# Kernel tuning notes

Measured on AMD Instinct MI355X. Metric: run time of the kernel, lower is better.

## Reference

```python
import jax, jax.numpy as jnp
import numpy as np

B, S, H, I, E = 1, 2048, 2048, 5632, 8
JITTER = 0.01
NEG = jnp.float32(-1e30)  # stands in for -inf; softmax prob underflows to 0


def setup_inputs() -> dict:
    key = jax.random.key(0)
    ks = jax.random.split(key, 5)
    return {
        "hidden_states": jax.random.normal(ks[0], (B, S, H), jnp.float32),
        "gate_w": jax.random.normal(ks[1], (E, H), jnp.float32) * 0.02,   # nn.Linear(H, E) weight
        "w1": jax.random.normal(ks[2], (E, I, H), jnp.float32) * 0.02,    # per-expert w1 weight [out=I, in=H]
        "w2": jax.random.normal(ks[3], (E, H, I), jnp.float32) * 0.02,    # per-expert w2 weight [out=H, in=I]
        "w3": jax.random.normal(ks[4], (E, I, H), jnp.float32) * 0.02,    # per-expert w3 weight [out=I, in=H]
    }


def _sparsemixer_top2(scores, jitter_eps):
    # masked_sampling_omp_inference: sparse-mixer top-2 routing
    top2, sel = jax.lax.top_k(scores, 2)                      # [T,2], [T,2]
    e = scores.shape[-1]
    # --- first expert multiplier ---
    m1 = top2[:, 0:1]                                         # [T,1]
    factor1 = jnp.maximum(jnp.abs(scores), m1)                # clamp(|s|, min=m1)
    mask1 = (m1 - scores) / factor1 > 2.0 * jitter_eps
    p1 = jax.nn.softmax(jnp.where(mask1, NEG, scores), axis=-1)
    mult1 = jnp.take_along_axis(p1, sel[:, 0:1], axis=-1)     # [T,1]
    # --- second expert multiplier (first expert knocked out) ---
    m2 = top2[:, 1:2]
    factor2 = jnp.maximum(jnp.abs(scores), m2)
    mask2 = (m2 - scores) / factor2 > 2.0 * jitter_eps
    onehot0 = sel[:, 0:1] == jnp.arange(e)[None, :]           # scatter(-inf) at top-1 index
    p2 = jax.nn.softmax(jnp.where(onehot0 | mask2, NEG, scores), axis=-1)
    mult2 = jnp.take_along_axis(p2, sel[:, 1:2], axis=-1)     # [T,1]
    return jnp.concatenate([mult1, mult2], axis=-1), sel       # [T,2], [T,2]


def reference(hidden_states, gate_w, w1, w2, w3):
    b, s, h = hidden_states.shape
    x = hidden_states.reshape(-1, h)                          # [T,H]
    logits = x @ gate_w.T                                     # [T,E] router logits
    mult, sel = _sparsemixer_top2(logits, JITTER)
    out = jnp.zeros_like(x)
    for e in range(w1.shape[0]):                              # fixed small expert count
        # combined routing weight for expert e (0 if not selected)
        we = jnp.sum(jnp.where(sel == e, mult, 0.0), axis=-1)  # [T]
        hid = jax.nn.silu(x @ w1[e].T) * (x @ w3[e].T)        # SwiGLU [T,I]
        out = out + we[:, None] * (hid @ w2[e].T)
    return out.reshape(b, s, h)
```

## Files before the change

### kernel.cpp

```cpp
#include <hip/hip_runtime.h>

#define TOKENS 2048
#define HDIM   2048
#define IDIM   5632
#define NEXP   8
#define NSLOT  (TOKENS * 2)
#define BM 128
#define BN 128
#define BK 32

typedef __attribute__((ext_vector_type(8))) short bf16x8;
typedef __attribute__((ext_vector_type(4))) float f32x4;

__device__ __forceinline__ unsigned short f2bf(float f) {
    union { float f; unsigned u; } v; v.f = f;
    unsigned r = v.u + 0x7FFFu + ((v.u >> 16) & 1u);
    return (unsigned short)(r >> 16);
}
__device__ __forceinline__ unsigned pack2(float lo, float hi) {
    return (unsigned)f2bf(lo) | ((unsigned)f2bf(hi) << 16);
}
__device__ __forceinline__ void stage_b_chunk(const float* __restrict__ p, unsigned short* dst) {
    float4 lo = *(const float4*)(p);
    float4 hi = *(const float4*)(p + 4);
    uint4 v;
    v.x = pack2(lo.x, lo.y);
    v.y = pack2(lo.z, lo.w);
    v.z = pack2(hi.x, hi.y);
    v.w = pack2(hi.z, hi.w);
    *(uint4*)dst = v;
}

__global__ __launch_bounds__(256) void k_zero(float* __restrict__ out) {
    int i = blockIdx.x * 256 + threadIdx.x;
    float4 z = {0.f, 0.f, 0.f, 0.f};
    ((float4*)out)[i] = z;
}

__global__ __launch_bounds__(256) void k_gate(const float* __restrict__ x,
                                              const float* __restrict__ gw,
                                              int* __restrict__ sel,
                                              float* __restrict__ wts) {
    int wave = threadIdx.x >> 6, lane = threadIdx.x & 63;
    int t = blockIdx.x * 4 + wave;
    const float4* xr = (const float4*)(x + (size_t)t * HDIM);
    const float4* g  = (const float4*)gw;
    float acc[NEXP];
#pragma unroll
    for (int e = 0; e < NEXP; e++) acc[e] = 0.f;
#pragma unroll
    for (int it = 0; it < HDIM / 4 / 64; ++it) {
        int idx = it * 64 + lane;
        float4 xv = xr[idx];
#pragma unroll
        for (int e = 0; e < NEXP; e++) {
            float4 gv = g[e * (HDIM / 4) + idx];
            acc[e] += xv.x * gv.x + xv.y * gv.y + xv.z * gv.z + xv.w * gv.w;
        }
    }
#pragma unroll
    for (int e = 0; e < NEXP; e++) {
        float v = acc[e];
#pragma unroll
        for (int off = 32; off > 0; off >>= 1) v += __shfl_xor(v, off, 64);
        acc[e] = v;
    }
    if (lane == 0) {
        float s[NEXP];
#pragma unroll
        for (int e = 0; e < NEXP; e++) s[e] = acc[e];
        float m1 = s[0]; int i1 = 0;
#pragma unroll
        for (int e = 1; e < NEXP; e++) if (s[e] > m1) { m1 = s[e]; i1 = e; }
        float m2 = -3.0e38f; int i2 = 0;
#pragma unroll
        for (int e = 0; e < NEXP; e++) if (e != i1 && s[e] > m2) { m2 = s[e]; i2 = e; }
        float sum1 = 0.f;
#pragma unroll
        for (int e = 0; e < NEXP; e++) {
            float f = fmaxf(fabsf(s[e]), m1);
            bool masked = ((m1 - s[e]) / f) > 0.02f;
            if (!masked) sum1 += expf(s[e] - m1);
        }
        float sum2 = 0.f;
#pragma unroll
        for (int e = 0; e < NEXP; e++) {
            if (e == i1) continue;
            float f = fmaxf(fabsf(s[e]), m2);
            bool masked = ((m2 - s[e]) / f) > 0.02f;
            if (!masked) sum2 += expf(s[e] - m2);
        }
        sel[2 * t]     = i1;
        sel[2 * t + 1] = i2;
        wts[2 * t]     = 1.f / sum1;
        wts[2 * t + 1] = 1.f / sum2;
    }
}

__global__ __launch_bounds__(256) void k_hist(const int* __restrict__ sel,
                                              int* __restrict__ cnt,
                                              int* __restrict__ offs,
                                              int* __restrict__ cursor) {
    __shared__ int c_s[NEXP];
    int tid = threadIdx.x;
    if (tid < NEXP) c_s[tid] = 0;
    __syncthreads();
    for (int i = tid; i < NSLOT; i += 256) atomicAdd(&c_s[sel[i]], 1);
    __syncthreads();
    if (tid == 0) {
        int o = 0;
        for (int e = 0; e < NEXP; e++) { cnt[e] = c_s[e]; offs[e] = o; o += c_s[e]; cursor[e] = 0; }
    }
}

__global__ __launch_bounds__(256) void k_gather(const float* __restrict__ x,
                                                const int* __restrict__ sel,
                                                const float* __restrict__ wts,
                                                const int* __restrict__ offs,
                                                int* __restrict__ cursor,
                                                int* __restrict__ rowtok,
                                                float* __restrict__ roww,
                                                unsigned short* __restrict__ Xe) {
    int t = blockIdx.x;
    __shared__ int slot_s[2];
    if (threadIdx.x == 0) {
        int s0 = sel[2 * t], s1 = sel[2 * t + 1];
        int p0 = offs[s0] + atomicAdd(&cursor[s0], 1);
        int p1 = offs[s1] + atomicAdd(&cursor[s1], 1);
        rowtok[p0] = t; roww[p0] = wts[2 * t];
        rowtok[p1] = t; roww[p1] = wts[2 * t + 1];
        slot_s[0] = p0; slot_s[1] = p1;
    }
    __syncthreads();
    int p0 = slot_s[0], p1 = slot_s[1];
    int base = threadIdx.x * 8;
    const float* xp = x + (size_t)t * HDIM + base;
    float4 a = *(const float4*)(xp);
    float4 b = *(const float4*)(xp + 4);
    uint4 v;
    v.x = pack2(a.x, a.y); v.y = pack2(a.z, a.w);
    v.z = pack2(b.x, b.y); v.w = pack2(b.z, b.w);
    *(uint4*)(Xe + (size_t)p0 * HDIM + base) = v;
    *(uint4*)(Xe + (size_t)p1 * HDIM + base) = v;
}

__global__ __launch_bounds__(256, 2) void k_ffn1(const unsigned short* __restrict__ Xe,
                                                 const float* __restrict__ w1,
                                                 const float* __restrict__ w3,
                                                 const int* __restrict__ cnt,
                                                 const int* __restrict__ offs,
                                                 unsigned short* __restrict__ hid) {
    int e = blockIdx.z;
    int c = cnt[e];
    int bm = blockIdx.y;
    if (bm * BM >= c) return;
    int n0 = blockIdx.x * BN;
    int row0 = offs[e] + bm * BM;
    int rows_here = c - bm * BM;
    const float* W1 = w1 + (size_t)e * IDIM * HDIM;
    const float* W3 = w3 + (size_t)e * IDIM * HDIM;

    __shared__ __align__(16) unsigned short As[8 * 512];
    __shared__ __align__(16) unsigned short B1s[8 * 512];
    __shared__ __align__(16) unsigned short B3s[8 * 512];

    int tid = threadIdx.x, lane = tid & 63, wave = tid >> 6;
    int wm = wave >> 1, wn = wave & 1;
    int fr = lane & 15, kq = lane >> 4;

    f32x4 acc1[4][4], acc3[4][4];
    f32x4 z = {0.f, 0.f, 0.f, 0.f};
#pragma unroll
    for (int i = 0; i < 4; i++)
#pragma unroll
        for (int j = 0; j < 4; j++) { acc1[i][j] = z; acc3[i][j] = z; }

    int ar0 = min(row0 + wave * 16 + fr, NSLOT - 1);
    int ar1 = min(row0 + (wave + 4) * 16 + fr, NSLOT - 1);
    const unsigned short* aP0 = Xe + (size_t)ar0 * HDIM + kq * 8;
    const unsigned short* aP1 = Xe + (size_t)ar1 * HDIM + kq * 8;
    const float* b1P0 = W1 + (size_t)(n0 + wave * 16 + fr) * HDIM + kq * 8;
    const float* b1P1 = W1 + (size_t)(n0 + (wave + 4) * 16 + fr) * HDIM + kq * 8;
    const float* b3P0 = W3 + (size_t)(n0 + wave * 16 + fr) * HDIM + kq * 8;
    const float* b3P1 = W3 + (size_t)(n0 + (wave + 4) * 16 + fr) * HDIM + kq * 8;

    for (int k0 = 0; k0 < HDIM; k0 += BK) {
        __syncthreads();
        *(uint4*)&As[(size_t)tid * 8]         = *(const uint4*)(aP0 + k0);
        *(uint4*)&As[(size_t)(tid + 256) * 8] = *(const uint4*)(aP1 + k0);
        stage_b_chunk(b1P0 + k0, &B1s[(size_t)tid * 8]);
        stage_b_chunk(b1P1 + k0, &B1s[(size_t)(tid + 256) * 8]);
        stage_b_chunk(b3P0 + k0, &B3s[(size_t)tid * 8]);
        stage_b_chunk(b3P1 + k0, &B3s[(size_t)(tid + 256) * 8]);
        __syncthreads();
        bf16x8 af[4];
#pragma unroll
        for (int i = 0; i < 4; i++)
            af[i] = *(const bf16x8*)&As[((wm * 4 + i) * 64 + lane) * 8];
#pragma unroll
        for (int j = 0; j < 4; j++) {
            bf16x8 b1f = *(const bf16x8*)&B1s[((wn * 4 + j) * 64 + lane) * 8];
            bf16x8 b3f = *(const bf16x8*)&B3s[((wn * 4 + j) * 64 + lane) * 8];
#pragma unroll
            for (int i = 0; i < 4; i++) {
                acc1[i][j] = __builtin_amdgcn_mfma_f32_16x16x32_bf16(af[i], b1f, acc1[i][j], 0, 0, 0);
                acc3[i][j] = __builtin_amdgcn_mfma_f32_16x16x32_bf16(af[i], b3f, acc3[i][j], 0, 0, 0);
            }
        }
    }
    int qr = (lane >> 4) * 4, cb = lane & 15;
#pragma unroll
    for (int i = 0; i < 4; i++) {
        int rl = wm * 64 + i * 16 + qr;
#pragma unroll
        for (int v = 0; v < 4; v++) {
            int r = rl + v;
            if (r < rows_here) {
                size_t rowoff = (size_t)(row0 + r) * IDIM;
#pragma unroll
                for (int j = 0; j < 4; j++) {
                    float u1 = acc1[i][j][v], u3 = acc3[i][j][v];
                    float h = u1 * u3 / (1.f + __expf(-u1));
                    hid[rowoff + n0 + wn * 64 + j * 16 + cb] = f2bf(h);
                }
            }
        }
    }
}

__global__ __launch_bounds__(256, 2) void k_ffn2(const unsigned short* __restrict__ hid,
                                                 const float* __restrict__ w2,
                                                 const int* __restrict__ cnt,
                                                 const int* __restrict__ offs,
                                                 const int* __restrict__ rowtok,
                                                 const float* __restrict__ roww,
                                                 float* __restrict__ out) {
    int e = blockIdx.z;
    int c = cnt[e];
    int bm = blockIdx.y;
    if (bm * BM >= c) return;
    int n0 = blockIdx.x * BN;
    int row0 = offs[e] + bm * BM;
    int rows_here = c - bm * BM;
    const float* W2 = w2 + (size_t)e * HDIM * IDIM;

    __shared__ __align__(16) unsigned short As[8 * 512];
    __shared__ __align__(16) unsigned short Bs[8 * 512];
    __shared__ int   tok_s[BM];
    __shared__ float w_s[BM];

    int tid = threadIdx.x, lane = tid & 63, wave = tid >> 6;
    int wm = wave >> 1, wn = wave & 1;
    int fr = lane & 15, kq = lane >> 4;

    if (tid < BM) {
        bool valid = (tid < rows_here);
        tok_s[tid] = valid ? rowtok[row0 + tid] : 0;
        w_s[tid]   = valid ? roww[row0 + tid] : 0.f;
    }

    f32x4 acc[4][4];
    f32x4 z = {0.f, 0.f, 0.f, 0.f};
#pragma unroll
    for (int i = 0; i < 4; i++)
#pragma unroll
        for (int j = 0; j < 4; j++) acc[i][j] = z;

    int ar0 = min(row0 + wave * 16 + fr, NSLOT - 1);
    int ar1 = min(row0 + (wave + 4) * 16 + fr, NSLOT - 1);
    const unsigned short* aP0 = hid + (size_t)ar0 * IDIM + kq * 8;
    const unsigned short* aP1 = hid + (size_t)ar1 * IDIM + kq * 8;
    const float* bP0 = W2 + (size_t)(n0 + wave * 16 + fr) * IDIM + kq * 8;
    const float* bP1 = W2 + (size_t)(n0 + (wave + 4) * 16 + fr) * IDIM + kq * 8;

    for (int k0 = 0; k0 < IDIM; k0 += BK) {
        __syncthreads();
        *(uint4*)&As[(size_t)tid * 8]         = *(const uint4*)(aP0 + k0);
        *(uint4*)&As[(size_t)(tid + 256) * 8] = *(const uint4*)(aP1 + k0);
        stage_b_chunk(bP0 + k0, &Bs[(size_t)tid * 8]);
        stage_b_chunk(bP1 + k0, &Bs[(size_t)(tid + 256) * 8]);
        __syncthreads();
        bf16x8 af[4];
#pragma unroll
        for (int i = 0; i < 4; i++)
            af[i] = *(const bf16x8*)&As[((wm * 4 + i) * 64 + lane) * 8];
#pragma unroll
        for (int j = 0; j < 4; j++) {
            bf16x8 bf = *(const bf16x8*)&Bs[((wn * 4 + j) * 64 + lane) * 8];
#pragma unroll
            for (int i = 0; i < 4; i++)
                acc[i][j] = __builtin_amdgcn_mfma_f32_16x16x32_bf16(af[i], bf, acc[i][j], 0, 0, 0);
        }
    }
    int qr = (lane >> 4) * 4, cb = lane & 15;
#pragma unroll
    for (int i = 0; i < 4; i++) {
        int rl = wm * 64 + i * 16 + qr;
#pragma unroll
        for (int v = 0; v < 4; v++) {
            int r = rl + v;
            if (r < rows_here) {
                int tok = tok_s[r];
                float wgt = w_s[r];
                float* orow = out + (size_t)tok * HDIM + n0 + wn * 64 + cb;
#pragma unroll
                for (int j = 0; j < 4; j++)
                    atomicAdd(orow + j * 16, acc[i][j][v] * wgt);
            }
        }
    }
}

extern "C" void kernel_launch(void* const* d_in, const int* in_sizes, int n_in,
                              void* d_out, int out_size, void* d_ws, size_t ws_size,
                              hipStream_t stream) {
    const float* x  = (const float*)d_in[0];
    const float* gw = (const float*)d_in[1];
    const float* w1 = (const float*)d_in[2];
    const float* w2 = (const float*)d_in[3];
    const float* w3 = (const float*)d_in[4];
    float* out = (float*)d_out;

    char* ws = (char*)d_ws;
    int*   sel    = (int*)(ws);
    float* wts    = (float*)(ws + 16 * 1024);
    int*   cnt    = (int*)(ws + 32 * 1024);
    int*   offs   = (int*)(ws + 32 * 1024 + 256);
    int*   cursor = (int*)(ws + 32 * 1024 + 512);
    int*   rowtok = (int*)(ws + 48 * 1024);
    float* roww   = (float*)(ws + 64 * 1024);
    unsigned short* Xe  = (unsigned short*)(ws + (1 << 20));
    unsigned short* hid = (unsigned short*)(ws + (1 << 20) + (size_t)NSLOT * HDIM * 2);

    k_zero<<<dim3((TOKENS * HDIM / 4) / 256), dim3(256), 0, stream>>>(out);
    k_gate<<<dim3(TOKENS / 4), dim3(256), 0, stream>>>(x, gw, sel, wts);
    k_hist<<<dim3(1), dim3(256), 0, stream>>>(sel, cnt, offs, cursor);
    k_gather<<<dim3(TOKENS), dim3(256), 0, stream>>>(x, sel, wts, offs, cursor, rowtok, roww, Xe);
    k_ffn1<<<dim3(IDIM / BN, TOKENS / BM, NEXP), dim3(256), 0, stream>>>(Xe, w1, w3, cnt, offs, hid);
    k_ffn2<<<dim3(HDIM / BN, TOKENS / BM, NEXP), dim3(256), 0, stream>>>(hid, w2, cnt, offs, rowtok, roww, out);
}
```

Baseline: 1.892 ms.

## Pre-convert expert weights to bf16 and load GEMM tiles directly into LDS

Adds a conversion pass that turns w1, w3 and w2 into bf16 in workspace once per call. The FFN GEMMs then stream those bf16 tiles into LDS with global_load_lds instead of converting fp32 on the fly. The second GEMM now writes weighted per-slot outputs and a separate combine kernel sums each token's two slots, replacing atomic adds and the zero pass. This costs extra full-weight read/write conversion traffic (~1.1 GB total) and a large workspace, and falls back to the old path if the workspace is too small.

```diff
diff --git a/kernel.cpp b/kernel.cpp
--- a/kernel.cpp
+++ b/kernel.cpp
@@ -30,11 +30,31 @@
     v.w = pack2(hi.z, hi.w);
     *(uint4*)dst = v;
 }
+__device__ __forceinline__ void gl2lds16(const void* g, void* l) {
+    __builtin_amdgcn_global_load_lds(
+        (const __attribute__((address_space(1))) unsigned int*)g,
+        (__attribute__((address_space(3))) unsigned int*)l,
+        16, 0, 0);
+}
 
 __global__ __launch_bounds__(256) void k_zero(float* __restrict__ out) {
     int i = blockIdx.x * 256 + threadIdx.x;
     float4 z = {0.f, 0.f, 0.f, 0.f};
     ((float4*)out)[i] = z;
+}
+
+__global__ __launch_bounds__(256) void k_cvt(const float* __restrict__ src,
+                                             unsigned short* __restrict__ dst,
+                                             int n8) {
+    int stride = gridDim.x * 256;
+    for (int i = blockIdx.x * 256 + threadIdx.x; i < n8; i += stride) {
+        const float4* p = (const float4*)(src + (size_t)i * 8);
+        float4 a = p[0], b = p[1];
+        uint4 v;
+        v.x = pack2(a.x, a.y); v.y = pack2(a.z, a.w);
+        v.z = pack2(b.x, b.y); v.w = pack2(b.z, b.w);
+        *(uint4*)(dst + (size_t)i * 8) = v;
+    }
 }
 
 __global__ __launch_bounds__(256) void k_gate(const float* __restrict__ x,
@@ -120,6 +140,7 @@
                                                 int* __restrict__ cursor,
                                                 int* __restrict__ rowtok,
                                                 float* __restrict__ roww,
+                                                int* __restrict__ tokslot,
                                                 unsigned short* __restrict__ Xe) {
     int t = blockIdx.x;
     __shared__ int slot_s[2];
@@ -129,6 +150,7 @@
         int p1 = offs[s1] + atomicAdd(&cursor[s1], 1);
         rowtok[p0] = t; roww[p0] = wts[2 * t];
         rowtok[p1] = t; roww[p1] = wts[2 * t + 1];
+        tokslot[2 * t] = p0; tokslot[2 * t + 1] = p1;
         slot_s[0] = p0; slot_s[1] = p1;
     }
     __syncthreads();
@@ -144,12 +166,202 @@
     *(uint4*)(Xe + (size_t)p1 * HDIM + base) = v;
 }
 
-__global__ __launch_bounds__(256, 2) void k_ffn1(const unsigned short* __restrict__ Xe,
-                                                 const float* __restrict__ w1,
-                                                 const float* __restrict__ w3,
-                                                 const int* __restrict__ cnt,
-                                                 const int* __restrict__ offs,
-                                                 unsigned short* __restrict__ hid) {
+
+__global__ __launch_bounds__(256, 2) void k_ffn1_bf(const unsigned short* __restrict__ Xe,
+                                                    const unsigned short* __restrict__ w1b,
+                                                    const unsigned short* __restrict__ w3b,
+                                                    const int* __restrict__ cnt,
+                                                    const int* __restrict__ offs,
+                                                    unsigned short* __restrict__ hid) {
+    int e = blockIdx.z;
+    int c = cnt[e];
+    int bm = blockIdx.y;
+    if (bm * BM >= c) return;
+    int n0 = blockIdx.x * BN;
+    int row0 = offs[e] + bm * BM;
+    int rows_here = c - bm * BM;
+    const unsigned short* W1 = w1b + (size_t)e * IDIM * HDIM;
+    const unsigned short* W3 = w3b + (size_t)e * IDIM * HDIM;
+
+    __shared__ __align__(16) unsigned short As[8 * 512];
+    __shared__ __align__(16) unsigned short B1s[8 * 512];
+    __shared__ __align__(16) unsigned short B3s[8 * 512];
+
+    int tid = threadIdx.x, lane = tid & 63, wave = tid >> 6;
+    int wm = wave >> 1, wn = wave & 1;
+    int fr = lane & 15, kq = lane >> 4;
+
+    f32x4 acc1[4][4], acc3[4][4];
+    f32x4 z = {0.f, 0.f, 0.f, 0.f};
+#pragma unroll
+    for (int i = 0; i < 4; i++)
+#pragma unroll
+        for (int j = 0; j < 4; j++) { acc1[i][j] = z; acc3[i][j] = z; }
+
+    int ar0 = min(row0 + wave * 16 + fr, NSLOT - 1);
+    int ar1 = min(row0 + (wave + 4) * 16 + fr, NSLOT - 1);
+    const unsigned short* aP0  = Xe + (size_t)ar0 * HDIM + kq * 8;
+    const unsigned short* aP1  = Xe + (size_t)ar1 * HDIM + kq * 8;
+    const unsigned short* b1P0 = W1 + (size_t)(n0 + wave * 16 + fr) * HDIM + kq * 8;
+    const unsigned short* b1P1 = W1 + (size_t)(n0 + (wave + 4) * 16 + fr) * HDIM + kq * 8;
+    const unsigned short* b3P0 = W3 + (size_t)(n0 + wave * 16 + fr) * HDIM + kq * 8;
+    const unsigned short* b3P1 = W3 + (size_t)(n0 + (wave + 4) * 16 + fr) * HDIM + kq * 8;
+
+    unsigned short* aL0  = As  + wave * 512;
+    unsigned short* aL1  = As  + (wave + 4) * 512;
+    unsigned short* b1L0 = B1s + wave * 512;
+    unsigned short* b1L1 = B1s + (wave + 4) * 512;
+    unsigned short* b3L0 = B3s + wave * 512;
+    unsigned short* b3L1 = B3s + (wave + 4) * 512;
+
+    for (int k0 = 0; k0 < HDIM; k0 += BK) {
+        __syncthreads();
+        gl2lds16(aP0 + k0, aL0);
+        gl2lds16(aP1 + k0, aL1);
+        gl2lds16(b1P0 + k0, b1L0);
+        gl2lds16(b1P1 + k0, b1L1);
+        gl2lds16(b3P0 + k0, b3L0);
+        gl2lds16(b3P1 + k0, b3L1);
+        __syncthreads();
+        bf16x8 af[4];
+#pragma unroll
+        for (int i = 0; i < 4; i++)
+            af[i] = *(const bf16x8*)&As[((wm * 4 + i) * 64 + lane) * 8];
+#pragma unroll
+        for (int j = 0; j < 4; j++) {
+            bf16x8 b1f = *(const bf16x8*)&B1s[((wn * 4 + j) * 64 + lane) * 8];
+            bf16x8 b3f = *(const bf16x8*)&B3s[((wn * 4 + j) * 64 + lane) * 8];
+#pragma unroll
+            for (int i = 0; i < 4; i++) {
+                acc1[i][j] = __builtin_amdgcn_mfma_f32_16x16x32_bf16(af[i], b1f, acc1[i][j], 0, 0, 0);
+                acc3[i][j] = __builtin_amdgcn_mfma_f32_16x16x32_bf16(af[i], b3f, acc3[i][j], 0, 0, 0);
+            }
+        }
+    }
+    int qr = (lane >> 4) * 4, cb = lane & 15;
+#pragma unroll
+    for (int i = 0; i < 4; i++) {
+        int rl = wm * 64 + i * 16 + qr;
+#pragma unroll
+        for (int v = 0; v < 4; v++) {
+            int r = rl + v;
+            if (r < rows_here) {
+                size_t rowoff = (size_t)(row0 + r) * IDIM;
+#pragma unroll
+                for (int j = 0; j < 4; j++) {
+                    float u1 = acc1[i][j][v], u3 = acc3[i][j][v];
+                    float h = u1 * u3 / (1.f + __expf(-u1));
+                    hid[rowoff + n0 + wn * 64 + j * 16 + cb] = f2bf(h);
+                }
+            }
+        }
+    }
+}
+
+__global__ __launch_bounds__(256, 2) void k_ffn2_bf(const unsigned short* __restrict__ hid,
+                                                    const unsigned short* __restrict__ w2b,
+                                                    const int* __restrict__ cnt,
+                                                    const int* __restrict__ offs,
+                                                    const float* __restrict__ roww,
+                                                    float* __restrict__ Oslot) {
+    int e = blockIdx.z;
+    int c = cnt[e];
+    int bm = blockIdx.y;
+    if (bm * BM >= c) return;
+    int n0 = blockIdx.x * BN;
+    int row0 = offs[e] + bm * BM;
+    int rows_here = c - bm * BM;
+    const unsigned short* W2 = w2b + (size_t)e * HDIM * IDIM;
+
+    __shared__ __align__(16) unsigned short As[8 * 512];
+    __shared__ __align__(16) unsigned short Bs[8 * 512];
+    __shared__ float w_s[BM];
+
+    int tid = threadIdx.x, lane = tid & 63, wave = tid >> 6;
+    int wm = wave >> 1, wn = wave & 1;
+    int fr = lane & 15, kq = lane >> 4;
+
+    if (tid < BM) w_s[tid] = (tid < rows_here) ? roww[row0 + tid] : 0.f;
+
+    f32x4 acc[4][4];
+    f32x4 z = {0.f, 0.f, 0.f, 0.f};
+#pragma unroll
+    for (int i = 0; i < 4; i++)
+#pragma unroll
+        for (int j = 0; j < 4; j++) acc[i][j] = z;
+
+    int ar0 = min(row0 + wave * 16 + fr, NSLOT - 1);
+    int ar1 = min(row0 + (wave + 4) * 16 + fr, NSLOT - 1);
+    const unsigned short* aP0 = hid + (size_t)ar0 * IDIM + kq * 8;
+    const unsigned short* aP1 = hid + (size_t)ar1 * IDIM + kq * 8;
+    const unsigned short* bP0 = W2 + (size_t)(n0 + wave * 16 + fr) * IDIM + kq * 8;
+    const unsigned short* bP1 = W2 + (size_t)(n0 + (wave + 4) * 16 + fr) * IDIM + kq * 8;
+
+    unsigned short* aL0 = As + wave * 512;
+    unsigned short* aL1 = As + (wave + 4) * 512;
+    unsigned short* bL0 = Bs + wave * 512;
+    unsigned short* bL1 = Bs + (wave + 4) * 512;
+
+    for (int k0 = 0; k0 < IDIM; k0 += BK) {
+        __syncthreads();
+        gl2lds16(aP0 + k0, aL0);
+        gl2lds16(aP1 + k0, aL1);
+        gl2lds16(bP0 + k0, bL0);
+        gl2lds16(bP1 + k0, bL1);
+        __syncthreads();
+        bf16x8 af[4];
+#pragma unroll
+        for (int i = 0; i < 4; i++)
+            af[i] = *(const bf16x8*)&As[((wm * 4 + i) * 64 + lane) * 8];
+#pragma unroll
+        for (int j = 0; j < 4; j++) {
+            bf16x8 bf = *(const bf16x8*)&Bs[((wn * 4 + j) * 64 + lane) * 8];
+#pragma unroll
+            for (int i = 0; i < 4; i++)
+                acc[i][j] = __builtin_amdgcn_mfma_f32_16x16x32_bf16(af[i], bf, acc[i][j], 0, 0, 0);
+        }
+    }
+    int qr = (lane >> 4) * 4, cb = lane & 15;
+#pragma unroll
+    for (int i = 0; i < 4; i++) {
+        int rl = wm * 64 + i * 16 + qr;
+#pragma unroll
+        for (int v = 0; v < 4; v++) {
+            int r = rl + v;
+            if (r < rows_here) {
+                float wgt = w_s[r];
+                float* orow = Oslot + (size_t)(row0 + r) * HDIM + n0 + wn * 64 + cb;
+#pragma unroll
+                for (int j = 0; j < 4; j++)
+                    orow[j * 16] = acc[i][j][v] * wgt;
+            }
+        }
+    }
+}
+
+__global__ __launch_bounds__(256) void k_combine(const float* __restrict__ Oslot,
+                                                 const int* __restrict__ tokslot,
+                                                 float* __restrict__ out) {
+    int t = blockIdx.x;
+    int p0 = tokslot[2 * t], p1 = tokslot[2 * t + 1];
+    int i = threadIdx.x * 8;
+    const float4* r0 = (const float4*)(Oslot + (size_t)p0 * HDIM + i);
+    const float4* r1 = (const float4*)(Oslot + (size_t)p1 * HDIM + i);
+    float4 a0 = r0[0], b0 = r0[1], a1 = r1[0], b1 = r1[1];
+    float4 o0 = {a0.x + a1.x, a0.y + a1.y, a0.z + a1.z, a0.w + a1.w};
+    float4 o1 = {b0.x + b1.x, b0.y + b1.y, b0.z + b1.z, b0.w + b1.w};
+    float* op = out + (size_t)t * HDIM + i;
+    *(float4*)op = o0;
+    *(float4*)(op + 4) = o1;
+}
+
+
+__global__ __launch_bounds__(256, 2) void k_ffn1_cv(const unsigned short* __restrict__ Xe,
+                                                    const float* __restrict__ w1,
+                                                    const float* __restrict__ w3,
+                                                    const int* __restrict__ cnt,
+                                                    const int* __restrict__ offs,
+                                                    unsigned short* __restrict__ hid) {
     int e = blockIdx.z;
     int c = cnt[e];
     int bm = blockIdx.y;
@@ -228,13 +440,13 @@
     }
 }
 
-__global__ __launch_bounds__(256, 2) void k_ffn2(const unsigned short* __restrict__ hid,
-                                                 const float* __restrict__ w2,
-                                                 const int* __restrict__ cnt,
-                                                 const int* __restrict__ offs,
-                                                 const int* __restrict__ rowtok,
-                                                 const float* __restrict__ roww,
-                                                 float* __restrict__ out) {
+__global__ __launch_bounds__(256, 2) void k_ffn2_cv(const unsigned short* __restrict__ hid,
+                                                    const float* __restrict__ w2,
+                                                    const int* __restrict__ cnt,
+                                                    const int* __restrict__ offs,
+                                                    const int* __restrict__ rowtok,
+                                                    const float* __restrict__ roww,
+                                                    float* __restrict__ out) {
     int e = blockIdx.z;
     int c = cnt[e];
     int bm = blockIdx.y;
@@ -322,20 +534,38 @@
     float* out = (float*)d_out;
 
     char* ws = (char*)d_ws;
-    int*   sel    = (int*)(ws);
-    float* wts    = (float*)(ws + 16 * 1024);
-    int*   cnt    = (int*)(ws + 32 * 1024);
-    int*   offs   = (int*)(ws + 32 * 1024 + 256);
-    int*   cursor = (int*)(ws + 32 * 1024 + 512);
-    int*   rowtok = (int*)(ws + 48 * 1024);
-    float* roww   = (float*)(ws + 64 * 1024);
-    unsigned short* Xe  = (unsigned short*)(ws + (1 << 20));
-    unsigned short* hid = (unsigned short*)(ws + (1 << 20) + (size_t)NSLOT * HDIM * 2);
-
-    k_zero<<<dim3((TOKENS * HDIM / 4) / 256), dim3(256), 0, stream>>>(out);
+    int*   sel     = (int*)(ws);
+    float* wts     = (float*)(ws + 16 * 1024);
+    int*   cnt     = (int*)(ws + 32 * 1024);
+    int*   offs    = (int*)(ws + 32 * 1024 + 256);
+    int*   cursor  = (int*)(ws + 32 * 1024 + 512);
+    int*   rowtok  = (int*)(ws + 48 * 1024);
+    float* roww    = (float*)(ws + 64 * 1024);
+    int*   tokslot = (int*)(ws + 80 * 1024);
+    unsigned short* Xe  = (unsigned short*)(ws + (1ull << 20));
+    unsigned short* hid = (unsigned short*)(ws + (18ull << 20));
+    float*          Osl = (float*)(ws + (64ull << 20));
+    unsigned short* w1b = (unsigned short*)(ws + (100ull << 20));
+    unsigned short* w3b = (unsigned short*)(ws + (290ull << 20));
+    unsigned short* w2b = w1b;
+
+    const size_t EIH = (size_t)NEXP * IDIM * HDIM;
+    const size_t REQ = (290ull << 20) + EIH * 2;
+
     k_gate<<<dim3(TOKENS / 4), dim3(256), 0, stream>>>(x, gw, sel, wts);
     k_hist<<<dim3(1), dim3(256), 0, stream>>>(sel, cnt, offs, cursor);
-    k_gather<<<dim3(TOKENS), dim3(256), 0, stream>>>(x, sel, wts, offs, cursor, rowtok, roww, Xe);
-    k_ffn1<<<dim3(IDIM / BN, TOKENS / BM, NEXP), dim3(256), 0, stream>>>(Xe, w1, w3, cnt, offs, hid);
-    k_ffn2<<<dim3(HDIM / BN, TOKENS / BM, NEXP), dim3(256), 0, stream>>>(hid, w2, cnt, offs, rowtok, roww, out);
-}
+    k_gather<<<dim3(TOKENS), dim3(256), 0, stream>>>(x, sel, wts, offs, cursor, rowtok, roww, tokslot, Xe);
+
+    if (ws_size >= REQ) {
+        k_cvt<<<dim3(2048), dim3(256), 0, stream>>>(w1, w1b, (int)(EIH / 8));
+        k_cvt<<<dim3(2048), dim3(256), 0, stream>>>(w3, w3b, (int)(EIH / 8));
+        k_ffn1_bf<<<dim3(IDIM / BN, TOKENS / BM, NEXP), dim3(256), 0, stream>>>(Xe, w1b, w3b, cnt, offs, hid);
+        k_cvt<<<dim3(2048), dim3(256), 0, stream>>>(w2, w2b, (int)(EIH / 8));
+        k_ffn2_bf<<<dim3(HDIM / BN, TOKENS / BM, NEXP), dim3(256), 0, stream>>>(hid, w2b, cnt, offs, roww, Osl);
+        k_combine<<<dim3(TOKENS), dim3(256), 0, stream>>>(Osl, tokslot, out);
+    } else {
+        k_zero<<<dim3((TOKENS * HDIM / 4) / 256), dim3(256), 0, stream>>>(out);
+        k_ffn1_cv<<<dim3(IDIM / BN, TOKENS / BM, NEXP), dim3(256), 0, stream>>>(Xe, w1, w3, cnt, offs, hid);
+        k_ffn2_cv<<<dim3(HDIM / BN, TOKENS / BM, NEXP), dim3(256), 0, stream>>>(hid, w2, cnt, offs, rowtok, roww, out);
+    }
+}
```

Measured after the change: 1.838 ms. 2.9% less time.
